# Kernel optimization log

Hardware: AMD Instinct MI355X
Metric: run time of the kernel (lower is better)

The kernel has to match this reference:

```python
import jax, jax.numpy as jnp
import numpy as np

B, N, S, D, H = 8, 64, 128, 512, 8
DK = D // H


def setup_inputs() -> dict:
    key = jax.random.key(0)
    ks = jax.random.split(key, 8)
    x = jax.random.normal(ks[0], (B, N, S, D), dtype=jnp.float32)
    mask = jax.random.randint(ks[1], (B, N, S), 0, 2).astype(jnp.int32)
    mask = mask.at[..., 0].set(1)  # guarantee at least one valid token per sentence
    w = 1.0 / np.sqrt(D).astype(np.float32)
    Wq = jax.random.normal(ks[2], (D, D), dtype=jnp.float32) * w
    Wk = jax.random.normal(ks[3], (D, D), dtype=jnp.float32) * w
    Wv = jax.random.normal(ks[4], (D, D), dtype=jnp.float32) * w
    Wo = jax.random.normal(ks[5], (D, D), dtype=jnp.float32) * w
    bq = jnp.zeros((D,), jnp.float32)
    bk = jnp.zeros((D,), jnp.float32)
    bv = jnp.zeros((D,), jnp.float32)
    bo = jnp.zeros((D,), jnp.float32)
    sent_q = jax.random.normal(ks[6], (H, DK), dtype=jnp.float32)
    return {"x": x, "mask": mask, "Wq": Wq, "bq": bq, "Wk": Wk, "bk": bk,
            "Wv": Wv, "bv": bv, "sent_q": sent_q, "Wo": Wo, "bo": bo}


def reference(x, mask, Wq, bq, Wk, bk, Wv, bv, sent_q, Wo, bo):
    b, n, s, d = x.shape
    h, dk = sent_q.shape
    inv_sqrt_dk = 1.0 / np.sqrt(dk).astype(np.float32)
    # QKV projections, split heads: (B, N, S, H, dk)
    Q = (x @ Wq + bq).reshape(b, n, s, h, dk)
    K = (x @ Wk + bk).reshape(b, n, s, h, dk)
    V = (x @ Wv + bv).reshape(b, n, s, h, dk)
    # sentence-query attention over tokens within each sentence: (B, H, N, S)
    sent_scores = jnp.einsum('hd,bnshd->bhns', sent_q, K) * inv_sqrt_dk
    sent_scores = jnp.where(mask[:, None, :, :] == 0, jnp.float32(-1e9), sent_scores)
    sent_attn = jax.nn.softmax(sent_scores, axis=-1)
    # pooled per-sentence representation: (B, H, N, dk)
    sent_repr = jnp.einsum('bhns,bnshd->bhnd', sent_attn, V)
    # degenerate token softmax over a single key (== 1), kept faithfully
    token_scores = jnp.einsum('bnshd,bhnd->bhns', Q, sent_repr) * inv_sqrt_dk
    token_attn = jax.nn.softmax(token_scores[..., None], axis=-1)[..., 0]  # (B,H,N,S), all ones
    # broadcast pooled repr to every token, scale by (unit) attn: (B, H, N, S, dk)
    out = token_attn[..., None] * sent_repr[:, :, :, None, :]
    out = jnp.transpose(out, (0, 2, 3, 1, 4)).reshape(b, n, s, d)
    return out @ Wo + bo
```

## Files before the change

kernel.cpp:

```cpp
#include <hip/hip_runtime.h>
#include <math.h>

#define BB 8
#define NN 64
#define SS 128
#define DD 512
#define HH 8
#define DKK 64
#define NSENT (BB * NN)
#define SENT_STRIDE (SS * DD)

#define WK_OFF 0
#define XB_OFF 4096
#define Z_OFF  (XB_OFF + NSENT * HH * DD)
#define YY_OFF (Z_OFF + NSENT * DD)

__global__ void precompute_wk(const float* __restrict__ Wk,
                              const float* __restrict__ sq,
                              float* __restrict__ wk_t) {
    const int d = threadIdx.x;
    const int h = blockIdx.x;
    const float4* wrow = (const float4*)(Wk + (size_t)d * DD + h * DKK);
    const float4* sqv  = (const float4*)(sq + h * DKK);
    float acc = 0.f;
#pragma unroll
    for (int k = 0; k < DKK / 4; ++k) {
        float4 w = wrow[k], q = sqv[k];
        acc += w.x * q.x + w.y * q.y + w.z * q.z + w.w * q.w;
    }
    wk_t[h * DD + d] = acc;
}

__global__ __launch_bounds__(512)
void ka_xbar(const float* __restrict__ x, const int* __restrict__ mask,
             const float* __restrict__ wk_t, float* __restrict__ xbar)
{
    __shared__ float wl[HH][SS];
    __shared__ float rsh[HH];

    const int sent = blockIdx.x;
    const int t    = threadIdx.x;
    const int wave = t >> 6;
    const int lane = t & 63;
    const float* xs = x + (size_t)sent * SENT_STRIDE;

    const int d0 = lane * 8;
    float4 wkA[HH], wkB[HH];
#pragma unroll
    for (int h = 0; h < HH; ++h) {
        wkA[h] = *(const float4*)(wk_t + h * DD + d0);
        wkB[h] = *(const float4*)(wk_t + h * DD + d0 + 4);
    }
    const int hsel = lane & 7;

    for (int j = 0; j < 16; j += 2) {
        const int s0 = wave * 16 + j;
        const float* xr0 = xs + (size_t)s0 * DD + d0;
        const float* xr1 = xr0 + DD;
        float4 xa0 = *(const float4*)xr0;
        float4 xb0 = *(const float4*)(xr0 + 4);
        float4 xa1 = *(const float4*)xr1;
        float4 xb1 = *(const float4*)(xr1 + 4);
        const int m0 = mask[sent * SS + s0];
        const int m1 = mask[sent * SS + s0 + 1];
        float p0[HH], p1[HH];
#pragma unroll
        for (int h = 0; h < HH; ++h) {
            p0[h] = xa0.x * wkA[h].x + xa0.y * wkA[h].y + xa0.z * wkA[h].z + xa0.w * wkA[h].w
                  + xb0.x * wkB[h].x + xb0.y * wkB[h].y + xb0.z * wkB[h].z + xb0.w * wkB[h].w;
            p1[h] = xa1.x * wkA[h].x + xa1.y * wkA[h].y + xa1.z * wkA[h].z + xa1.w * wkA[h].w
                  + xb1.x * wkB[h].x + xb1.y * wkB[h].y + xb1.z * wkB[h].z + xb1.w * wkB[h].w;
        }
#pragma unroll
        for (int off = 1; off <= 4; off <<= 1) {
#pragma unroll
            for (int h = 0; h < HH; ++h) {
                p0[h] += __shfl_xor(p0[h], off, 64);
                p1[h] += __shfl_xor(p1[h], off, 64);
            }
        }
        float v0 = p0[0], v1 = p1[0];
#pragma unroll
        for (int h = 1; h < HH; ++h) {
            v0 = (hsel == h) ? p0[h] : v0;
            v1 = (hsel == h) ? p1[h] : v1;
        }
#pragma unroll
        for (int off = 8; off <= 32; off <<= 1) {
            v0 += __shfl_xor(v0, off, 64);
            v1 += __shfl_xor(v1, off, 64);
        }
        if (lane < HH) {
            wl[lane][s0]     = m0 ? __expf(v0 * 0.125f) : 0.f;
            wl[lane][s0 + 1] = m1 ? __expf(v1 * 0.125f) : 0.f;
        }
    }
    __syncthreads();

    {
        float v = wl[wave][lane] + wl[wave][lane + 64];
#pragma unroll
        for (int off = 1; off <= 32; off <<= 1)
            v += __shfl_xor(v, off, 64);
        if (lane == 0) rsh[wave] = 1.0f / v;
    }
    __syncthreads();

    {
        const float* xp = xs + t;
        float acc[HH];
#pragma unroll
        for (int h = 0; h < HH; ++h) acc[h] = 0.f;

        float xa[8], xb[8];
#pragma unroll
        for (int j = 0; j < 8; ++j) xa[j] = xp[(size_t)j * DD];

        for (int s0 = 0; s0 < SS; s0 += 16) {
#pragma unroll
            for (int j = 0; j < 8; ++j) xb[j] = xp[(size_t)(s0 + 8 + j) * DD];
#pragma unroll
            for (int j = 0; j < 8; ++j) {
                const float xv = xa[j];
#pragma unroll
                for (int h = 0; h < HH; ++h) acc[h] += wl[h][s0 + j] * xv;
            }
            if (s0 + 16 < SS) {
#pragma unroll
                for (int j = 0; j < 8; ++j) xa[j] = xp[(size_t)(s0 + 16 + j) * DD];
            }
#pragma unroll
            for (int j = 0; j < 8; ++j) {
                const float xv = xb[j];
#pragma unroll
                for (int h = 0; h < HH; ++h) acc[h] += wl[h][s0 + 8 + j] * xv;
            }
        }
        float* xbp = xbar + (size_t)sent * (HH * DD) + t;
#pragma unroll
        for (int h = 0; h < HH; ++h)
            xbp[h * DD] = acc[h] * rsh[h];
    }
}

__global__ __launch_bounds__(256)
void gemm_tile(const float* __restrict__ A, const int am_stride, const int a_nb_stride,
               const float* __restrict__ B, const float* __restrict__ bias,
               float* __restrict__ C)
{
    __shared__ float As[64][17];
    __shared__ float Bs[64][68];

    const int nb = blockIdx.x & 7, mb = blockIdx.x >> 3;
    const int t  = threadIdx.x;
    const int tr = t >> 4, tc = t & 15;

    const float* Ab = A + (size_t)(mb * 16) * am_stride + nb * a_nb_stride
                        + (size_t)tr * am_stride + tc * 4;
    const float* Bb = B + nb * 64 + (size_t)tr * DD + tc * 4;

    float4 ar = *(const float4*)(Ab);
    float4 br0 = *(const float4*)(Bb);
    float4 br1 = *(const float4*)(Bb + 16 * DD);
    float4 br2 = *(const float4*)(Bb + 32 * DD);
    float4 br3 = *(const float4*)(Bb + 48 * DD);

    float a0 = 0.f, a1 = 0.f, a2 = 0.f, a3 = 0.f;

    for (int k0 = 0; k0 < DD; k0 += 64) {
        As[tc * 4 + 0][tr] = ar.x;
        As[tc * 4 + 1][tr] = ar.y;
        As[tc * 4 + 2][tr] = ar.z;
        As[tc * 4 + 3][tr] = ar.w;
        *(float4*)&Bs[tr +  0][tc * 4] = br0;
        *(float4*)&Bs[tr + 16][tc * 4] = br1;
        *(float4*)&Bs[tr + 32][tc * 4] = br2;
        *(float4*)&Bs[tr + 48][tc * 4] = br3;
        __syncthreads();
        if (k0 + 64 < DD) {
            ar  = *(const float4*)(Ab + k0 + 64);
            br0 = *(const float4*)(Bb + (size_t)(k0 + 64) * DD);
            br1 = *(const float4*)(Bb + (size_t)(k0 + 80) * DD);
            br2 = *(const float4*)(Bb + (size_t)(k0 + 96) * DD);
            br3 = *(const float4*)(Bb + (size_t)(k0 + 112) * DD);
        }
#pragma unroll
        for (int kk = 0; kk < 64; ++kk) {
            const float av = As[kk][tr];
            const float4 bv4 = *(const float4*)&Bs[kk][tc * 4];
            a0 += av * bv4.x; a1 += av * bv4.y; a2 += av * bv4.z; a3 += av * bv4.w;
        }
        __syncthreads();
    }

    const float4 bb = *(const float4*)(bias + nb * 64 + tc * 4);
    float4 o; o.x = a0 + bb.x; o.y = a1 + bb.y; o.z = a2 + bb.z; o.w = a3 + bb.w;
    *(float4*)(C + (size_t)(mb * 16 + tr) * DD + nb * 64 + tc * 4) = o;
}

__global__ __launch_bounds__(256)
void kb_bcast(const float* __restrict__ y, float* __restrict__ outp)
{
    const int sent = blockIdx.x >> 2, q = blockIdx.x & 3;
    const int c4 = threadIdx.x & 127;
    const int rr = threadIdx.x >> 7;
    const float4 yv = *(const float4*)(y + (size_t)sent * DD + c4 * 4);
    float* w0 = outp + (size_t)sent * SENT_STRIDE + (size_t)(q * 32 + rr) * DD + c4 * 4;
#pragma unroll
    for (int i = 0; i < 16; ++i)
        *(float4*)(w0 + (size_t)(i * 2) * DD) = yv;
}

extern "C" void kernel_launch(void* const* d_in, const int* in_sizes, int n_in,
                              void* d_out, int out_size, void* d_ws, size_t ws_size,
                              hipStream_t stream) {
    const float* x    = (const float*)d_in[0];
    const int*   mask = (const int*)  d_in[1];
    const float* Wk   = (const float*)d_in[4];
    const float* Wv   = (const float*)d_in[6];
    const float* bv   = (const float*)d_in[7];
    const float* sq   = (const float*)d_in[8];
    const float* Wo   = (const float*)d_in[9];
    const float* bo   = (const float*)d_in[10];
    float* out = (float*)d_out;
    float* ws  = (float*)d_ws;

    float* wk_t = ws + WK_OFF;
    float* xbar = ws + XB_OFF;
    float* z    = ws + Z_OFF;
    float* y    = ws + YY_OFF;

    precompute_wk<<<HH, DD, 0, stream>>>(Wk, sq, wk_t);
    ka_xbar<<<NSENT, 512, 0, stream>>>(x, mask, wk_t, xbar);
    gemm_tile<<<256, 256, 0, stream>>>(xbar, HH * DD, DD, Wv, bv, z);
    gemm_tile<<<256, 256, 0, stream>>>(z, DD, 0, Wo, bo, y);
    kb_bcast<<<NSENT * 4, 256, 0, stream>>>(y, out);
}
```

Before: 104.0 us.

## Fuse score and weighted-sum passes into single-read x kernel with DPP reductions

Replaces the two-pass per-sentence kernel, which read x once for scores and again for the weighted sum, with a single pass. Each wave handles 32 tokens and accumulates unnormalized exp-weighted x per head in registers, then combines the four waves' partials through shared memory. Cross-lane sums use DPP row rotations and ds_swizzle broadcasts, and the mask is read once via ballot. This halves global reads of x but raises register pressure (64 accumulator floats per thread) and shrinks blocks to 256 threads.

```diff
diff --git a/kernel.cpp b/kernel.cpp
--- a/kernel.cpp
+++ b/kernel.cpp
@@ -15,6 +15,24 @@
 #define Z_OFF  (XB_OFF + NSENT * HH * DD)
 #define YY_OFF (Z_OFF + NSENT * DD)
 
+template <int CTRL>
+__device__ __forceinline__ float ror_add(float v) {
+    int r = __builtin_amdgcn_update_dpp(0, __float_as_int(v), CTRL, 0xf, 0xf, true);
+    return v + __int_as_float(r);
+}
+__device__ __forceinline__ float row_allreduce(float v) {
+    v = ror_add<0x121>(v);
+    v = ror_add<0x122>(v);
+    v = ror_add<0x124>(v);
+    v = ror_add<0x128>(v);
+    return v;
+}
+template <int H>
+__device__ __forceinline__ float bcast8(float v) {
+    return __int_as_float(
+        __builtin_amdgcn_ds_swizzle(__float_as_int(v), (H << 5) | 0x18));
+}
+
 __global__ void precompute_wk(const float* __restrict__ Wk,
                               const float* __restrict__ sq,
                               float* __restrict__ wk_t) {
@@ -31,115 +49,138 @@
     wk_t[h * DD + d] = acc;
 }
 
-__global__ __launch_bounds__(512)
-void ka_xbar(const float* __restrict__ x, const int* __restrict__ mask,
-             const float* __restrict__ wk_t, float* __restrict__ xbar)
+__global__ __launch_bounds__(256, 2)
+void ka_fused(const float* __restrict__ x, const int* __restrict__ mask,
+              const float* __restrict__ wk_t, float* __restrict__ xbar)
 {
-    __shared__ float wl[HH][SS];
+    __shared__ float buf[2][HH][DD];
+    __shared__ float wsb[4][HH];
     __shared__ float rsh[HH];
 
     const int sent = blockIdx.x;
     const int t    = threadIdx.x;
     const int wave = t >> 6;
     const int lane = t & 63;
-    const float* xs = x + (size_t)sent * SENT_STRIDE;
-
-    const int d0 = lane * 8;
+    const int d0   = lane * 8;
+
     float4 wkA[HH], wkB[HH];
 #pragma unroll
     for (int h = 0; h < HH; ++h) {
         wkA[h] = *(const float4*)(wk_t + h * DD + d0);
         wkB[h] = *(const float4*)(wk_t + h * DD + d0 + 4);
     }
-    const int hsel = lane & 7;
-
-    for (int j = 0; j < 16; j += 2) {
-        const int s0 = wave * 16 + j;
-        const float* xr0 = xs + (size_t)s0 * DD + d0;
-        const float* xr1 = xr0 + DD;
-        float4 xa0 = *(const float4*)xr0;
-        float4 xb0 = *(const float4*)(xr0 + 4);
-        float4 xa1 = *(const float4*)xr1;
-        float4 xb1 = *(const float4*)(xr1 + 4);
-        const int m0 = mask[sent * SS + s0];
-        const int m1 = mask[sent * SS + s0 + 1];
+
+    const int mv = (lane < 32) ? mask[sent * SS + wave * 32 + lane] : 0;
+    const unsigned long long mb = __ballot(mv != 0);
+
+    float4 accA[HH], accB[HH];
+    float ws[HH];
+#pragma unroll
+    for (int h = 0; h < HH; ++h) {
+        accA[h] = make_float4(0.f, 0.f, 0.f, 0.f);
+        accB[h] = make_float4(0.f, 0.f, 0.f, 0.f);
+        ws[h] = 0.f;
+    }
+
+    const float* xp = x + (size_t)sent * SENT_STRIDE + (size_t)(wave * 32) * DD + d0;
+
+    float4 a0 = *(const float4*)(xp);
+    float4 b0 = *(const float4*)(xp + 4);
+    float4 a1 = *(const float4*)(xp + DD);
+    float4 b1 = *(const float4*)(xp + DD + 4);
+
+#pragma unroll 4
+    for (int jp = 0; jp < 16; ++jp) {
+        float4 na0, nb0, na1, nb1;
+        if (jp < 15) {
+            const float* q = xp + (size_t)(2 * jp + 2) * DD;
+            na0 = *(const float4*)(q);
+            nb0 = *(const float4*)(q + 4);
+            na1 = *(const float4*)(q + DD);
+            nb1 = *(const float4*)(q + DD + 4);
+        }
+
         float p0[HH], p1[HH];
 #pragma unroll
         for (int h = 0; h < HH; ++h) {
-            p0[h] = xa0.x * wkA[h].x + xa0.y * wkA[h].y + xa0.z * wkA[h].z + xa0.w * wkA[h].w
-                  + xb0.x * wkB[h].x + xb0.y * wkB[h].y + xb0.z * wkB[h].z + xb0.w * wkB[h].w;
-            p1[h] = xa1.x * wkA[h].x + xa1.y * wkA[h].y + xa1.z * wkA[h].z + xa1.w * wkA[h].w
-                  + xb1.x * wkB[h].x + xb1.y * wkB[h].y + xb1.z * wkB[h].z + xb1.w * wkB[h].w;
-        }
-#pragma unroll
-        for (int off = 1; off <= 4; off <<= 1) {
-#pragma unroll
-            for (int h = 0; h < HH; ++h) {
-                p0[h] += __shfl_xor(p0[h], off, 64);
-                p1[h] += __shfl_xor(p1[h], off, 64);
-            }
-        }
+            p0[h] = a0.x * wkA[h].x + a0.y * wkA[h].y + a0.z * wkA[h].z + a0.w * wkA[h].w
+                  + b0.x * wkB[h].x + b0.y * wkB[h].y + b0.z * wkB[h].z + b0.w * wkB[h].w;
+            p1[h] = a1.x * wkA[h].x + a1.y * wkA[h].y + a1.z * wkA[h].z + a1.w * wkA[h].w
+                  + b1.x * wkB[h].x + b1.y * wkB[h].y + b1.z * wkB[h].z + b1.w * wkB[h].w;
+        }
+#pragma unroll
+        for (int h = 0; h < HH; ++h) {
+            p0[h] = row_allreduce(p0[h]);
+            p1[h] = row_allreduce(p1[h]);
+        }
+        const int r = lane & 7;
         float v0 = p0[0], v1 = p1[0];
 #pragma unroll
         for (int h = 1; h < HH; ++h) {
-            v0 = (hsel == h) ? p0[h] : v0;
-            v1 = (hsel == h) ? p1[h] : v1;
-        }
-#pragma unroll
-        for (int off = 8; off <= 32; off <<= 1) {
-            v0 += __shfl_xor(v0, off, 64);
-            v1 += __shfl_xor(v1, off, 64);
-        }
-        if (lane < HH) {
-            wl[lane][s0]     = m0 ? __expf(v0 * 0.125f) : 0.f;
-            wl[lane][s0 + 1] = m1 ? __expf(v1 * 0.125f) : 0.f;
-        }
+            v0 = (r == h) ? p0[h] : v0;
+            v1 = (r == h) ? p1[h] : v1;
+        }
+        v0 += __shfl_xor(v0, 16, 64);
+        v0 += __shfl_xor(v0, 32, 64);
+        v1 += __shfl_xor(v1, 16, 64);
+        v1 += __shfl_xor(v1, 32, 64);
+
+        const float e0 = ((mb >> (2 * jp)) & 1)     ? __expf(v0 * 0.125f) : 0.f;
+        const float e1 = ((mb >> (2 * jp + 1)) & 1) ? __expf(v1 * 0.125f) : 0.f;
+
+#define ACC_H(H)                                                              \
+        {                                                                     \
+            const float e0h = bcast8<H>(e0);                                  \
+            const float e1h = bcast8<H>(e1);                                  \
+            accA[H].x += e0h * a0.x + e1h * a1.x;                             \
+            accA[H].y += e0h * a0.y + e1h * a1.y;                             \
+            accA[H].z += e0h * a0.z + e1h * a1.z;                             \
+            accA[H].w += e0h * a0.w + e1h * a1.w;                             \
+            accB[H].x += e0h * b0.x + e1h * b1.x;                             \
+            accB[H].y += e0h * b0.y + e1h * b1.y;                             \
+            accB[H].z += e0h * b0.z + e1h * b1.z;                             \
+            accB[H].w += e0h * b0.w + e1h * b1.w;                             \
+            ws[H] += e0h + e1h;                                               \
+        }
+        ACC_H(0) ACC_H(1) ACC_H(2) ACC_H(3) ACC_H(4) ACC_H(5) ACC_H(6) ACC_H(7)
+#undef ACC_H
+
+        if (jp < 15) { a0 = na0; b0 = nb0; a1 = na1; b1 = nb1; }
+    }
+
+    if (wave >= 2) {
+#pragma unroll
+        for (int h = 0; h < HH; ++h) {
+            *(float4*)&buf[wave - 2][h][d0]     = accA[h];
+            *(float4*)&buf[wave - 2][h][d0 + 4] = accB[h];
+        }
+    }
+    if (lane == 0) {
+#pragma unroll
+        for (int h = 0; h < HH; ++h) wsb[wave][h] = ws[h];
     }
     __syncthreads();
-
-    {
-        float v = wl[wave][lane] + wl[wave][lane + 64];
-#pragma unroll
-        for (int off = 1; off <= 32; off <<= 1)
-            v += __shfl_xor(v, off, 64);
-        if (lane == 0) rsh[wave] = 1.0f / v;
-    }
+    if (wave < 2) {
+#pragma unroll
+        for (int h = 0; h < HH; ++h) {
+            float4 u = *(const float4*)&buf[wave][h][d0];
+            float4 w2 = *(const float4*)&buf[wave][h][d0 + 4];
+            u.x += accA[h].x;  u.y += accA[h].y;  u.z += accA[h].z;  u.w += accA[h].w;
+            w2.x += accB[h].x; w2.y += accB[h].y; w2.z += accB[h].z; w2.w += accB[h].w;
+            *(float4*)&buf[wave][h][d0]     = u;
+            *(float4*)&buf[wave][h][d0 + 4] = w2;
+        }
+    }
+    if (t < HH)
+        rsh[t] = 1.0f / (wsb[0][t] + wsb[1][t] + wsb[2][t] + wsb[3][t]);
     __syncthreads();
 
-    {
-        const float* xp = xs + t;
-        float acc[HH];
-#pragma unroll
-        for (int h = 0; h < HH; ++h) acc[h] = 0.f;
-
-        float xa[8], xb[8];
-#pragma unroll
-        for (int j = 0; j < 8; ++j) xa[j] = xp[(size_t)j * DD];
-
-        for (int s0 = 0; s0 < SS; s0 += 16) {
-#pragma unroll
-            for (int j = 0; j < 8; ++j) xb[j] = xp[(size_t)(s0 + 8 + j) * DD];
-#pragma unroll
-            for (int j = 0; j < 8; ++j) {
-                const float xv = xa[j];
-#pragma unroll
-                for (int h = 0; h < HH; ++h) acc[h] += wl[h][s0 + j] * xv;
-            }
-            if (s0 + 16 < SS) {
-#pragma unroll
-                for (int j = 0; j < 8; ++j) xa[j] = xp[(size_t)(s0 + 16 + j) * DD];
-            }
-#pragma unroll
-            for (int j = 0; j < 8; ++j) {
-                const float xv = xb[j];
-#pragma unroll
-                for (int h = 0; h < HH; ++h) acc[h] += wl[h][s0 + 8 + j] * xv;
-            }
-        }
-        float* xbp = xbar + (size_t)sent * (HH * DD) + t;
-#pragma unroll
-        for (int h = 0; h < HH; ++h)
-            xbp[h * DD] = acc[h] * rsh[h];
+    float* xbp = xbar + (size_t)sent * (HH * DD);
+#pragma unroll
+    for (int h = 0; h < HH; ++h) {
+        const float r1 = rsh[h];
+        xbp[h * DD + t]       = (buf[0][h][t]       + buf[1][h][t])       * r1;
+        xbp[h * DD + t + 256] = (buf[0][h][t + 256] + buf[1][h][t + 256]) * r1;
     }
 }
 
@@ -231,7 +272,7 @@
     float* y    = ws + YY_OFF;
 
     precompute_wk<<<HH, DD, 0, stream>>>(Wk, sq, wk_t);
-    ka_xbar<<<NSENT, 512, 0, stream>>>(x, mask, wk_t, xbar);
+    ka_fused<<<NSENT, 256, 0, stream>>>(x, mask, wk_t, xbar);
     gemm_tile<<<256, 256, 0, stream>>>(xbar, HH * DD, DD, Wv, bv, z);
     gemm_tile<<<256, 256, 0, stream>>>(z, DD, 0, Wo, bo, y);
     kb_bcast<<<NSENT * 4, 256, 0, stream>>>(y, out);
```

Measured after the change: 120.6 us. 1.16x slower.

## Split score and pooling passes; fuse output projection with broadcast

Applied to the files above, without the earlier changes.

The per-sentence attention kernel is split in two. One kernel computes masked exp scores per token, using DPP row reductions in place of shuffles. A second kernel uses four blocks per sentence to pool x and folds the softmax normalization into a running weight sum. The Wo projection GEMM is fused with the broadcast store, which removes the separate y buffer and one launch. The split raises parallelism but reads x from memory twice, and the fused kernel writes the whole output with only 256 blocks.

```diff
diff --git a/kernel.cpp b/kernel.cpp
--- a/kernel.cpp
+++ b/kernel.cpp
@@ -8,12 +8,26 @@
 #define HH 8
 #define DKK 64
 #define NSENT (BB * NN)
+#define NTOK  (NSENT * SS)
 #define SENT_STRIDE (SS * DD)
 
 #define WK_OFF 0
-#define XB_OFF 4096
-#define Z_OFF  (XB_OFF + NSENT * HH * DD)
-#define YY_OFF (Z_OFF + NSENT * DD)
+#define W_OFF  4096
+#define Z_OFF  4096
+#define XB_OFF (W_OFF + NTOK * HH)
+
+template <int CTRL>
+__device__ __forceinline__ float ror_add(float v) {
+    int r = __builtin_amdgcn_update_dpp(0, __float_as_int(v), CTRL, 0xf, 0xf, true);
+    return v + __int_as_float(r);
+}
+__device__ __forceinline__ float row_allreduce(float v) {
+    v = ror_add<0x121>(v);
+    v = ror_add<0x122>(v);
+    v = ror_add<0x124>(v);
+    v = ror_add<0x128>(v);
+    return v;
+}
 
 __global__ void precompute_wk(const float* __restrict__ Wk,
                               const float* __restrict__ sq,
@@ -31,116 +45,132 @@
     wk_t[h * DD + d] = acc;
 }
 
-__global__ __launch_bounds__(512)
-void ka_xbar(const float* __restrict__ x, const int* __restrict__ mask,
-             const float* __restrict__ wk_t, float* __restrict__ xbar)
+__global__ __launch_bounds__(256, 4)
+void ks_scores(const float* __restrict__ x, const int* __restrict__ mask,
+               const float* __restrict__ wk_t, float* __restrict__ w)
 {
-    __shared__ float wl[HH][SS];
-    __shared__ float rsh[HH];
-
-    const int sent = blockIdx.x;
     const int t    = threadIdx.x;
     const int wave = t >> 6;
     const int lane = t & 63;
-    const float* xs = x + (size_t)sent * SENT_STRIDE;
-
-    const int d0 = lane * 8;
+    const int d0   = lane * 8;
+    const int tok0 = blockIdx.x * 8 + wave * 2;
+
+    const float* xp = x + (size_t)tok0 * DD + d0;
+    const float4 a0 = *(const float4*)(xp);
+    const float4 b0 = *(const float4*)(xp + 4);
+    const float4 a1 = *(const float4*)(xp + DD);
+    const float4 b1 = *(const float4*)(xp + DD + 4);
+
     float4 wkA[HH], wkB[HH];
 #pragma unroll
     for (int h = 0; h < HH; ++h) {
         wkA[h] = *(const float4*)(wk_t + h * DD + d0);
         wkB[h] = *(const float4*)(wk_t + h * DD + d0 + 4);
     }
-    const int hsel = lane & 7;
-
-    for (int j = 0; j < 16; j += 2) {
-        const int s0 = wave * 16 + j;
-        const float* xr0 = xs + (size_t)s0 * DD + d0;
-        const float* xr1 = xr0 + DD;
-        float4 xa0 = *(const float4*)xr0;
-        float4 xb0 = *(const float4*)(xr0 + 4);
-        float4 xa1 = *(const float4*)xr1;
-        float4 xb1 = *(const float4*)(xr1 + 4);
-        const int m0 = mask[sent * SS + s0];
-        const int m1 = mask[sent * SS + s0 + 1];
-        float p0[HH], p1[HH];
-#pragma unroll
-        for (int h = 0; h < HH; ++h) {
-            p0[h] = xa0.x * wkA[h].x + xa0.y * wkA[h].y + xa0.z * wkA[h].z + xa0.w * wkA[h].w
-                  + xb0.x * wkB[h].x + xb0.y * wkB[h].y + xb0.z * wkB[h].z + xb0.w * wkB[h].w;
-            p1[h] = xa1.x * wkA[h].x + xa1.y * wkA[h].y + xa1.z * wkA[h].z + xa1.w * wkA[h].w
-                  + xb1.x * wkB[h].x + xb1.y * wkB[h].y + xb1.z * wkB[h].z + xb1.w * wkB[h].w;
-        }
-#pragma unroll
-        for (int off = 1; off <= 4; off <<= 1) {
-#pragma unroll
-            for (int h = 0; h < HH; ++h) {
-                p0[h] += __shfl_xor(p0[h], off, 64);
-                p1[h] += __shfl_xor(p1[h], off, 64);
-            }
-        }
-        float v0 = p0[0], v1 = p1[0];
-#pragma unroll
-        for (int h = 1; h < HH; ++h) {
-            v0 = (hsel == h) ? p0[h] : v0;
-            v1 = (hsel == h) ? p1[h] : v1;
-        }
-#pragma unroll
-        for (int off = 8; off <= 32; off <<= 1) {
-            v0 += __shfl_xor(v0, off, 64);
-            v1 += __shfl_xor(v1, off, 64);
-        }
-        if (lane < HH) {
-            wl[lane][s0]     = m0 ? __expf(v0 * 0.125f) : 0.f;
-            wl[lane][s0 + 1] = m1 ? __expf(v1 * 0.125f) : 0.f;
-        }
+    const int m0 = mask[tok0];
+    const int m1 = mask[tok0 + 1];
+
+    float p0[HH], p1[HH];
+#pragma unroll
+    for (int h = 0; h < HH; ++h) {
+        p0[h] = a0.x * wkA[h].x + a0.y * wkA[h].y + a0.z * wkA[h].z + a0.w * wkA[h].w
+              + b0.x * wkB[h].x + b0.y * wkB[h].y + b0.z * wkB[h].z + b0.w * wkB[h].w;
+        p1[h] = a1.x * wkA[h].x + a1.y * wkA[h].y + a1.z * wkA[h].z + a1.w * wkA[h].w
+              + b1.x * wkB[h].x + b1.y * wkB[h].y + b1.z * wkB[h].z + b1.w * wkB[h].w;
+    }
+#pragma unroll
+    for (int h = 0; h < HH; ++h) {
+        p0[h] = row_allreduce(p0[h]);
+        p1[h] = row_allreduce(p1[h]);
+    }
+    const int r = lane & 7;
+    float v0 = p0[0], v1 = p1[0];
+#pragma unroll
+    for (int h = 1; h < HH; ++h) {
+        v0 = (r == h) ? p0[h] : v0;
+        v1 = (r == h) ? p1[h] : v1;
+    }
+    v0 += __shfl_xor(v0, 16, 64);
+    v0 += __shfl_xor(v0, 32, 64);
+    v1 += __shfl_xor(v1, 16, 64);
+    v1 += __shfl_xor(v1, 32, 64);
+
+    const float e0 = m0 ? __expf(v0 * 0.125f) : 0.f;
+    const float e1 = m1 ? __expf(v1 * 0.125f) : 0.f;
+
+    if (lane < 16) {
+        const float e = (lane < 8) ? e0 : e1;
+        w[(size_t)tok0 * HH + lane] = e;
+    }
+}
+
+__global__ __launch_bounds__(128, 8)
+void kx_xbar(const float* __restrict__ x, const float* __restrict__ w,
+             float* __restrict__ xbar)
+{
+    __shared__ float wl[SS][HH];
+
+    const int bid  = blockIdx.x;
+    const int sent = bid >> 2, q = bid & 3;
+    const int t    = threadIdx.x;
+
+    {
+        const float4* wp = (const float4*)(w + (size_t)sent * SS * HH);
+        const float4 w0 = wp[t * 2];
+        const float4 w1 = wp[t * 2 + 1];
+        *(float4*)&wl[t][0] = w0;
+        *(float4*)&wl[t][4] = w1;
     }
     __syncthreads();
 
-    {
-        float v = wl[wave][lane] + wl[wave][lane + 64];
-#pragma unroll
-        for (int off = 1; off <= 32; off <<= 1)
-            v += __shfl_xor(v, off, 64);
-        if (lane == 0) rsh[wave] = 1.0f / v;
-    }
-    __syncthreads();
-
-    {
-        const float* xp = xs + t;
-        float acc[HH];
-#pragma unroll
-        for (int h = 0; h < HH; ++h) acc[h] = 0.f;
-
-        float xa[8], xb[8];
-#pragma unroll
-        for (int j = 0; j < 8; ++j) xa[j] = xp[(size_t)j * DD];
-
-        for (int s0 = 0; s0 < SS; s0 += 16) {
-#pragma unroll
-            for (int j = 0; j < 8; ++j) xb[j] = xp[(size_t)(s0 + 8 + j) * DD];
-#pragma unroll
-            for (int j = 0; j < 8; ++j) {
-                const float xv = xa[j];
-#pragma unroll
-                for (int h = 0; h < HH; ++h) acc[h] += wl[h][s0 + j] * xv;
-            }
-            if (s0 + 16 < SS) {
-#pragma unroll
-                for (int j = 0; j < 8; ++j) xa[j] = xp[(size_t)(s0 + 16 + j) * DD];
-            }
-#pragma unroll
-            for (int j = 0; j < 8; ++j) {
-                const float xv = xb[j];
-#pragma unroll
-                for (int h = 0; h < HH; ++h) acc[h] += wl[h][s0 + 8 + j] * xv;
-            }
-        }
-        float* xbp = xbar + (size_t)sent * (HH * DD) + t;
-#pragma unroll
-        for (int h = 0; h < HH; ++h)
-            xbp[h * DD] = acc[h] * rsh[h];
-    }
+    const int d = q * 128 + t;
+    const float* xp = x + (size_t)sent * SENT_STRIDE + d;
+
+    float acc[HH], wsum[HH];
+#pragma unroll
+    for (int h = 0; h < HH; ++h) { acc[h] = 0.f; wsum[h] = 0.f; }
+
+    float xa[8], xb[8];
+#pragma unroll
+    for (int j = 0; j < 8; ++j) xa[j] = xp[(size_t)j * DD];
+
+    for (int s0 = 0; s0 < SS; s0 += 16) {
+#pragma unroll
+        for (int j = 0; j < 8; ++j) xb[j] = xp[(size_t)(s0 + 8 + j) * DD];
+#pragma unroll
+        for (int j = 0; j < 8; ++j) {
+            const float4 w0 = *(const float4*)&wl[s0 + j][0];
+            const float4 w1 = *(const float4*)&wl[s0 + j][4];
+            const float xv = xa[j];
+            acc[0] += w0.x * xv; acc[1] += w0.y * xv;
+            acc[2] += w0.z * xv; acc[3] += w0.w * xv;
+            acc[4] += w1.x * xv; acc[5] += w1.y * xv;
+            acc[6] += w1.z * xv; acc[7] += w1.w * xv;
+            wsum[0] += w0.x; wsum[1] += w0.y; wsum[2] += w0.z; wsum[3] += w0.w;
+            wsum[4] += w1.x; wsum[5] += w1.y; wsum[6] += w1.z; wsum[7] += w1.w;
+        }
+        if (s0 + 16 < SS) {
+#pragma unroll
+            for (int j = 0; j < 8; ++j) xa[j] = xp[(size_t)(s0 + 16 + j) * DD];
+        }
+#pragma unroll
+        for (int j = 0; j < 8; ++j) {
+            const float4 w0 = *(const float4*)&wl[s0 + 8 + j][0];
+            const float4 w1 = *(const float4*)&wl[s0 + 8 + j][4];
+            const float xv = xb[j];
+            acc[0] += w0.x * xv; acc[1] += w0.y * xv;
+            acc[2] += w0.z * xv; acc[3] += w0.w * xv;
+            acc[4] += w1.x * xv; acc[5] += w1.y * xv;
+            acc[6] += w1.z * xv; acc[7] += w1.w * xv;
+            wsum[0] += w0.x; wsum[1] += w0.y; wsum[2] += w0.z; wsum[3] += w0.w;
+            wsum[4] += w1.x; wsum[5] += w1.y; wsum[6] += w1.z; wsum[7] += w1.w;
+        }
+    }
+
+    float* xbp = xbar + (size_t)sent * (HH * DD) + d;
+#pragma unroll
+    for (int h = 0; h < HH; ++h)
+        xbp[h * DD] = acc[h] / wsum[h];
 }
 
 __global__ __launch_bounds__(256)
@@ -199,16 +229,61 @@
 }
 
 __global__ __launch_bounds__(256)
-void kb_bcast(const float* __restrict__ y, float* __restrict__ outp)
+void kyb_proj_bcast(const float* __restrict__ z, const float* __restrict__ Wo,
+                    const float* __restrict__ bo, float* __restrict__ outp)
 {
-    const int sent = blockIdx.x >> 2, q = blockIdx.x & 3;
-    const int c4 = threadIdx.x & 127;
-    const int rr = threadIdx.x >> 7;
-    const float4 yv = *(const float4*)(y + (size_t)sent * DD + c4 * 4);
-    float* w0 = outp + (size_t)sent * SENT_STRIDE + (size_t)(q * 32 + rr) * DD + c4 * 4;
-#pragma unroll
-    for (int i = 0; i < 16; ++i)
-        *(float4*)(w0 + (size_t)(i * 2) * DD) = yv;
+    __shared__ float As[64][17];
+    __shared__ float Bs[64][68];
+
+    const int nb = blockIdx.x & 7, mb = blockIdx.x >> 3;
+    const int t  = threadIdx.x;
+    const int tr = t >> 4, tc = t & 15;
+
+    const float* Ab = z + (size_t)(mb * 16 + tr) * DD + tc * 4;
+    const float* Bb = Wo + nb * 64 + (size_t)tr * DD + tc * 4;
+
+    float4 ar = *(const float4*)(Ab);
+    float4 br0 = *(const float4*)(Bb);
+    float4 br1 = *(const float4*)(Bb + 16 * DD);
+    float4 br2 = *(const float4*)(Bb + 32 * DD);
+    float4 br3 = *(const float4*)(Bb + 48 * DD);
+
+    float a0 = 0.f, a1 = 0.f, a2 = 0.f, a3 = 0.f;
+
+    for (int k0 = 0; k0 < DD; k0 += 64) {
+        As[tc * 4 + 0][tr] = ar.x;
+        As[tc * 4 + 1][tr] = ar.y;
+        As[tc * 4 + 2][tr] = ar.z;
+        As[tc * 4 + 3][tr] = ar.w;
+        *(float4*)&Bs[tr +  0][tc * 4] = br0;
+        *(float4*)&Bs[tr + 16][tc * 4] = br1;
+        *(float4*)&Bs[tr + 32][tc * 4] = br2;
+        *(float4*)&Bs[tr + 48][tc * 4] = br3;
+        __syncthreads();
+        if (k0 + 64 < DD) {
+            ar  = *(const float4*)(Ab + k0 + 64);
+            br0 = *(const float4*)(Bb + (size_t)(k0 + 64) * DD);
+            br1 = *(const float4*)(Bb + (size_t)(k0 + 80) * DD);
+            br2 = *(const float4*)(Bb + (size_t)(k0 + 96) * DD);
+            br3 = *(const float4*)(Bb + (size_t)(k0 + 112) * DD);
+        }
+#pragma unroll
+        for (int kk = 0; kk < 64; ++kk) {
+            const float av = As[kk][tr];
+            const float4 bv4 = *(const float4*)&Bs[kk][tc * 4];
+            a0 += av * bv4.x; a1 += av * bv4.y; a2 += av * bv4.z; a3 += av * bv4.w;
+        }
+        __syncthreads();
+    }
+
+    const float4 bb = *(const float4*)(bo + nb * 64 + tc * 4);
+    float4 o; o.x = a0 + bb.x; o.y = a1 + bb.y; o.z = a2 + bb.z; o.w = a3 + bb.w;
+
+    const int sent = mb * 16 + tr;
+    float* op = outp + (size_t)sent * SENT_STRIDE + nb * 64 + tc * 4;
+#pragma unroll 8
+    for (int s = 0; s < SS; ++s)
+        *(float4*)(op + (size_t)s * DD) = o;
 }
 
 extern "C" void kernel_launch(void* const* d_in, const int* in_sizes, int n_in,
@@ -226,13 +301,13 @@
     float* ws  = (float*)d_ws;
 
     float* wk_t = ws + WK_OFF;
+    float* w    = ws + W_OFF;
     float* xbar = ws + XB_OFF;
     float* z    = ws + Z_OFF;
-    float* y    = ws + YY_OFF;
 
     precompute_wk<<<HH, DD, 0, stream>>>(Wk, sq, wk_t);
-    ka_xbar<<<NSENT, 512, 0, stream>>>(x, mask, wk_t, xbar);
+    ks_scores<<<NTOK / 8, 256, 0, stream>>>(x, mask, wk_t, w);
+    kx_xbar<<<NSENT * 4, 128, 0, stream>>>(x, w, xbar);
     gemm_tile<<<256, 256, 0, stream>>>(xbar, HH * DD, DD, Wv, bv, z);
-    gemm_tile<<<256, 256, 0, stream>>>(z, DD, 0, Wo, bo, y);
-    kb_bcast<<<NSENT * 4, 256, 0, stream>>>(y, out);
-}
+    kyb_proj_bcast<<<256, 256, 0, stream>>>(z, Wo, bo, out);
+}
```

New measurement: 135.0 us. 29.8% more time.
